# Optimization experiments

Measured on AMD Instinct MI355X. Metric: run time of the kernel, lower is better.

Reference implementation:

```python
import jax, jax.numpy as jnp
import numpy as np

N, F, T, H = 1024, 22, 1000, 64
EPS = 1e-5


def setup_inputs() -> dict:
    key = jax.random.key(0)
    ks = iter(jax.random.split(key, 64))
    def rn(shape, s=0.1):
        return jax.random.normal(next(ks), shape, jnp.float32) * s
    inp = {"x": rn((N, F, T), 1.0)}
    in_dims = [F, H, H]
    for l in range(3):
        inp[f"Wih{l}"] = rn((4 * H, in_dims[l]))
        inp[f"Whh{l}"] = rn((4 * H, H))
        inp[f"bih{l}"] = rn((4 * H,))
        inp[f"bhh{l}"] = rn((4 * H,))
    fc = [(64, 54), (54, 44), (44, 24), (24, 4)]
    for i, (di, do) in enumerate(fc):
        inp[f"w{i}"] = rn((do, di))
        inp[f"b{i}"] = rn((do,))
    for i, d in enumerate([54, 44, 24]):
        inp[f"g{i}"] = jnp.ones((d,), jnp.float32)
        inp[f"be{i}"] = jnp.zeros((d,), jnp.float32)
        inp[f"m{i}"] = rn((d,))
        inp[f"v{i}"] = jax.random.uniform(next(ks), (d,), jnp.float32) + 0.5
    return inp


def _lstm_layer(xs, Wih, Whh, b):
    # xs: (T, N, in) -> hs: (T, N, H)
    n = xs.shape[1]
    h0 = jnp.zeros((n, Whh.shape[1]), xs.dtype)
    def step(carry, xt):
        h, c = carry
        z = xt @ Wih.T + h @ Whh.T + b  # (N, 4H)
        i, f, g, o = jnp.split(z, 4, axis=-1)  # PyTorch gate order i,f,g,o
        c = jax.nn.sigmoid(f) * c + jax.nn.sigmoid(i) * jnp.tanh(g)
        h = jax.nn.sigmoid(o) * jnp.tanh(c)
        return (h, c), h
    (_, _), hs = jax.lax.scan(step, (h0, h0), xs)
    return hs


def _bn(x, g, be, m, v):
    return (x - m) * jax.lax.rsqrt(v + EPS) * g + be


def reference(x, Wih0, Whh0, bih0, bhh0, Wih1, Whh1, bih1, bhh1,
              Wih2, Whh2, bih2, bhh2,
              w0, b0, g0, be0, m0, v0,
              w1, b1, g1, be1, m1, v1,
              w2, b2, g2, be2, m2, v2,
              w3, b3):
    # (N, F, T) -> permute(0,2,1) -> (N, T, F); scan over time-major (T, N, F)
    xs = jnp.transpose(x, (2, 0, 1))
    xs = _lstm_layer(xs, Wih0, Whh0, bih0 + bhh0)
    xs = _lstm_layer(xs, Wih1, Whh1, bih1 + bhh1)
    xs = _lstm_layer(xs, Wih2, Whh2, bih2 + bhh2)
    h = xs[-1]  # last timestep, (N, H)
    h = jax.nn.relu(_bn(h @ w0.T + b0, g0, be0, m0, v0))
    h = jax.nn.relu(_bn(h @ w1.T + b1, g1, be1, m1, v1))
    h = jax.nn.relu(_bn(h @ w2.T + b2, g2, be2, m2, v2))
    return h @ w3.T + b3
```

## Files before the change

kernel.cpp:

```cpp
#include <hip/hip_runtime.h>
#include <hip/hip_fp16.h>

#define TT 1000
#define FF 22
#define HH 64
#define BB 4
#define NBLK 256
#define S0 112
#define S1 144
#define SL0 (4 * S0)
#define SL1 (4 * S1)

typedef _Float16 half8 __attribute__((ext_vector_type(8)));
typedef float float4v __attribute__((ext_vector_type(4)));

__device__ __forceinline__ float sigm(float v) {
    return __builtin_amdgcn_rcpf(1.0f + __expf(-v));
}
__device__ __forceinline__ float tanh_(float v) {
    return 1.0f - 2.0f * __builtin_amdgcn_rcpf(__expf(2.0f * v) + 1.0f);
}

__device__ __forceinline__ float sel4(const float4v a, int q) {
    float lo = (q & 2) ? a[2] : a[0];
    float hi = (q & 2) ? a[3] : a[1];
    return (q & 1) ? hi : lo;
}

__device__ __forceinline__ float gate_update(const float z[4], float& c) {
    float cc = sigm(z[1]) * c + sigm(z[0]) * tanh_(z[2]);
    c = cc;
    return sigm(z[3]) * tanh_(cc);
}

__device__ __forceinline__ int ldmin4(const int* p) {
    int4 v = *(const int4*)p;
    return min(min(v.x, v.y), min(v.z, v.w));
}

#define SPIN(cond) do { for (;;) { asm volatile("" ::: "memory"); if (cond) break; \
                        __builtin_amdgcn_s_sleep(1); } asm volatile("" ::: "memory"); } while (0)

extern "C" __global__ void __launch_bounds__(896, 1)
lstm_fused(const float* __restrict__ x,
           const float* __restrict__ Wih0, const float* __restrict__ Whh0,
           const float* __restrict__ bih0, const float* __restrict__ bhh0,
           const float* __restrict__ Wih1, const float* __restrict__ Whh1,
           const float* __restrict__ bih1, const float* __restrict__ bhh1,
           const float* __restrict__ Wih2, const float* __restrict__ Whh2,
           const float* __restrict__ bih2, const float* __restrict__ bhh2,
           const float* __restrict__ w0, const float* __restrict__ b0,
           const float* __restrict__ w1, const float* __restrict__ b1,
           const float* __restrict__ w2, const float* __restrict__ b2,
           const float* __restrict__ w3, const float* __restrict__ b3,
           const float* __restrict__ g0, const float* __restrict__ be0,
           const float* __restrict__ m0, const float* __restrict__ v0,
           const float* __restrict__ g1, const float* __restrict__ be1,
           const float* __restrict__ m1, const float* __restrict__ v1,
           const float* __restrict__ g2, const float* __restrict__ be2,
           const float* __restrict__ m2, const float* __restrict__ v2,
           float* __restrict__ out)
{
    __shared__ __align__(16) _Float16 in0[8 * SL0];
    __shared__ __align__(16) _Float16 in1[8 * SL1];
    __shared__ __align__(16) _Float16 in2[8 * SL1];
    __shared__ __align__(16) int flags[16];
    __shared__ float fcA[BB * 64];
    __shared__ float fcB[BB * 64];
    __shared__ float fcW[54 * 65];
    __shared__ float fcP[5 * 64];

    const int tid  = threadIdx.x;
    const int wv   = tid >> 6;
    const int role = wv >> 2;
    const int w4   = wv & 3;
    const int l    = tid & 63;
    const int q    = l >> 4;
    const int l15  = l & 15;
    const int u    = 16 * w4 + l15;
    const int b    = q;
    const int n0   = blockIdx.x * BB;

    for (int i = tid; i < 8 * SL0; i += 896) in0[i] = (_Float16)0.0f;
    for (int i = tid; i < 8 * SL1; i += 896) in1[i] = (_Float16)0.0f;
    for (int i = tid; i < 8 * SL1; i += 896) in2[i] = (_Float16)0.0f;
    if (tid < 16) flags[tid] = (tid >= 14) ? (1 << 29) : -1;

    half8 wf[4][4];
    float4v biasC[4];
    if (role == 2) {
#pragma unroll
        for (int g = 0; g < 4; ++g) {
            const int row = 64 * g + u;
#pragma unroll
            for (int kt = 0; kt < 3; ++kt) {
                half8 h{};
#pragma unroll
                for (int j = 0; j < 8; ++j) {
                    const int k = 32 * kt + 8 * q + j;
                    float val = 0.0f;
                    if (k < 32) { if (k < FF) val = Wih0[row * FF + k]; }
                    else        { val = Whh0[row * HH + (k - 32)]; }
                    h[j] = (_Float16)val;
                }
                wf[g][kt] = h;
            }
            float bv = bih0[row] + bhh0[row];
            biasC[g] = float4v{bv, bv, bv, bv};
        }
    } else if (role < 2) {
        const float* Wih = role ? Wih1 : Wih2;
        const float* Whh = role ? Whh1 : Whh2;
        const float* bih = role ? bih1 : bih2;
        const float* bhh = role ? bhh1 : bhh2;
#pragma unroll
        for (int g = 0; g < 4; ++g) {
            const int row = 64 * g + u;
#pragma unroll
            for (int kt = 0; kt < 4; ++kt) {
                half8 h{};
#pragma unroll
                for (int j = 0; j < 8; ++j) {
                    const int k = 32 * kt + 8 * q + j;
                    h[j] = (_Float16)((k < 64) ? Wih[row * HH + k] : Whh[row * HH + (k - 64)]);
                }
                wf[g][kt] = h;
            }
            float bv = bih[row] + bhh[row];
            biasC[g] = float4v{bv, bv, bv, bv};
        }
    }

    const int  st  = tid - 768;
    const bool xok = (role == 3) && (st >= 0) && (st < BB * FF);
    const int  xb  = xok ? (st / FF) : 0;
    const int  xf  = xok ? (st - xb * FF) : 0;
    const float* xp = x + ((size_t)(n0 + xb) * FF + xf) * TT;

    volatile int* vfl = (volatile int*)flags;
    __syncthreads();

    const int arow = (role == 2) ? ((l15 & 3) * S0 + q * 8) : ((l15 & 3) * S1 + q * 8);
    float c = 0.f;

    if (role == 3) {
        float xh = xok ? xp[0] : 0.f;
        for (int k = 0; k < 125; ++k) {
            const int tb = k * 8;
#pragma unroll
            for (int s = 0; s < 8; ++s) {
                const int t = tb + s;
                if ((s & 3) == 0) SPIN(ldmin4(flags + 8) >= t - 5);
                if (xok) in0[s * SL0 + xb * S0 + xf] = (_Float16)xh;
                __threadfence_block();
                if (l == 0) vfl[12 + (wv - 12)] = t;
                if (xok) xh = xp[(t + 1 < TT) ? (t + 1) : (TT - 1)];
            }
        }
    } else if (role == 2) {
        for (int k = 0; k < 125; ++k) {
            const int tb = k * 8;
#pragma unroll
            for (int s = 0; s < 8; ++s) {
                const int t = tb + s;
                if ((s & 3) == 0)
                    SPIN(ldmin4(flags + 12) >= t + 3 && ldmin4(flags + 4) >= t - 5);
                SPIN(ldmin4(flags + 8) >= t - 1);
                const _Float16* rd = in0 + s * SL0;
                half8 a0 = *(const half8*)(rd + arow);
                half8 a1 = *(const half8*)(rd + arow + 32);
                half8 a2 = *(const half8*)(rd + arow + 64);
                float4v acc[4];
#pragma unroll
                for (int g = 0; g < 4; ++g)
                    acc[g] = __builtin_amdgcn_mfma_f32_16x16x32_f16(a0, wf[g][0], biasC[g], 0, 0, 0);
#pragma unroll
                for (int g = 0; g < 4; ++g)
                    acc[g] = __builtin_amdgcn_mfma_f32_16x16x32_f16(a1, wf[g][1], acc[g], 0, 0, 0);
#pragma unroll
                for (int g = 0; g < 4; ++g)
                    acc[g] = __builtin_amdgcn_mfma_f32_16x16x32_f16(a2, wf[g][2], acc[g], 0, 0, 0);
                float z[4];
#pragma unroll
                for (int g = 0; g < 4; ++g) z[g] = sel4(acc[g], q);
                float h = gate_update(z, c);
                _Float16 hf = (_Float16)h;
                in0[((s + 1) & 7) * SL0 + b * S0 + 32 + u] = hf;
                in1[s * SL1 + b * S1 + u]                  = hf;
                __threadfence_block();
                if (l == 0) vfl[8 + w4] = t;
            }
        }
    } else {
        _Float16* rin  = role ? in1 : in2;
        _Float16* rout = role ? in2 : nullptr;
        const int* pin = role ? (flags + 8) : (flags + 4);
        const int* pow_ = role ? (flags + 4) : (flags + 0);
        for (int k = 0; k < 125; ++k) {
            const int tb = k * 8;
#pragma unroll
            for (int s = 0; s < 8; ++s) {
                const int t = tb + s;
                if ((s & 3) == 0) {
                    if (role) SPIN(ldmin4(pin) >= t + 3 && ldmin4(flags + 0) >= t - 5);
                    else      SPIN(ldmin4(pin) >= t + 3);
                }
                SPIN(ldmin4(pow_) >= t - 1);
                const _Float16* rd = rin + s * SL1;
                half8 a0 = *(const half8*)(rd + arow);
                half8 a1 = *(const half8*)(rd + arow + 32);
                half8 a2 = *(const half8*)(rd + arow + 64);
                half8 a3 = *(const half8*)(rd + arow + 96);
                float4v acc[4];
#pragma unroll
                for (int g = 0; g < 4; ++g)
                    acc[g] = __builtin_amdgcn_mfma_f32_16x16x32_f16(a0, wf[g][0], biasC[g], 0, 0, 0);
#pragma unroll
                for (int g = 0; g < 4; ++g)
                    acc[g] = __builtin_amdgcn_mfma_f32_16x16x32_f16(a1, wf[g][1], acc[g], 0, 0, 0);
#pragma unroll
                for (int g = 0; g < 4; ++g)
                    acc[g] = __builtin_amdgcn_mfma_f32_16x16x32_f16(a2, wf[g][2], acc[g], 0, 0, 0);
#pragma unroll
                for (int g = 0; g < 4; ++g)
                    acc[g] = __builtin_amdgcn_mfma_f32_16x16x32_f16(a3, wf[g][3], acc[g], 0, 0, 0);
                float z[4];
#pragma unroll
                for (int g = 0; g < 4; ++g) z[g] = sel4(acc[g], q);
                float h = gate_update(z, c);
                _Float16 hf = (_Float16)h;
                if (role) {
                    rin[((s + 1) & 7) * SL1 + b * S1 + 64 + u] = hf;
                    rout[s * SL1 + b * S1 + u]                 = hf;
                } else {
                    if (t != TT - 1) rin[((s + 1) & 7) * SL1 + b * S1 + 64 + u] = hf;
                    else             fcA[b * 64 + u] = h;
                }
                __threadfence_block();
                if (l == 0) vfl[(role ? 4 : 0) + w4] = t;
            }
        }
    }

    __syncthreads();

    for (int i = tid; i < 54 * 64; i += 896) fcW[(i >> 6) * 65 + (i & 63)] = w0[i];
    for (int i = tid; i < 54; i += 896) {
        fcP[i] = b0[i]; fcP[64 + i] = g0[i]; fcP[128 + i] = be0[i];
        fcP[192 + i] = m0[i]; fcP[256 + i] = v0[i];
    }
    __syncthreads();
    for (int idx = tid; idx < BB * 54; idx += 896) {
        const int bb = idx / 54, j = idx - bb * 54;
        float s = fcP[j];
        for (int k = 0; k < 64; ++k) s += fcW[j * 65 + k] * fcA[bb * 64 + k];
        s = (s - fcP[192 + j]) * rsqrtf(fcP[256 + j] + 1e-5f) * fcP[64 + j] + fcP[128 + j];
        fcB[bb * 64 + j] = fmaxf(s, 0.0f);
    }
    __syncthreads();

    for (int i = tid; i < 44 * 54; i += 896) fcW[(i / 54) * 55 + (i % 54)] = w1[i];
    for (int i = tid; i < 44; i += 896) {
        fcP[i] = b1[i]; fcP[64 + i] = g1[i]; fcP[128 + i] = be1[i];
        fcP[192 + i] = m1[i]; fcP[256 + i] = v1[i];
    }
    __syncthreads();
    for (int idx = tid; idx < BB * 44; idx += 896) {
        const int bb = idx / 44, j = idx - bb * 44;
        float s = fcP[j];
        for (int k = 0; k < 54; ++k) s += fcW[j * 55 + k] * fcB[bb * 64 + k];
        s = (s - fcP[192 + j]) * rsqrtf(fcP[256 + j] + 1e-5f) * fcP[64 + j] + fcP[128 + j];
        fcA[bb * 64 + j] = fmaxf(s, 0.0f);
    }
    __syncthreads();

    for (int i = tid; i < 24 * 44; i += 896) fcW[(i / 44) * 45 + (i % 44)] = w2[i];
    for (int i = tid; i < 24; i += 896) {
        fcP[i] = b2[i]; fcP[64 + i] = g2[i]; fcP[128 + i] = be2[i];
        fcP[192 + i] = m2[i]; fcP[256 + i] = v2[i];
    }
    __syncthreads();
    for (int idx = tid; idx < BB * 24; idx += 896) {
        const int bb = idx / 24, j = idx - bb * 24;
        float s = fcP[j];
        for (int k = 0; k < 44; ++k) s += fcW[j * 45 + k] * fcA[bb * 64 + k];
        s = (s - fcP[192 + j]) * rsqrtf(fcP[256 + j] + 1e-5f) * fcP[64 + j] + fcP[128 + j];
        fcB[bb * 64 + j] = fmaxf(s, 0.0f);
    }
    __syncthreads();

    for (int i = tid; i < 4 * 24; i += 896) fcW[(i / 24) * 25 + (i % 24)] = w3[i];
    for (int i = tid; i < 4; i += 896) fcP[i] = b3[i];
    __syncthreads();
    for (int idx = tid; idx < BB * 4; idx += 896) {
        const int bb = idx / 4, j = idx - bb * 4;
        float s = fcP[j];
        for (int k = 0; k < 24; ++k) s += fcW[j * 25 + k] * fcB[bb * 64 + k];
        out[(size_t)(n0 + bb) * 4 + j] = s;
    }
}

extern "C" void kernel_launch(void* const* d_in, const int* in_sizes, int n_in,
                              void* d_out, int out_size, void* d_ws, size_t ws_size,
                              hipStream_t stream) {
    const float* p[33];
    for (int i = 0; i < 33; ++i) p[i] = (const float*)d_in[i];
    lstm_fused<<<NBLK, 896, 0, stream>>>(
        p[0],
        p[1], p[2], p[3], p[4],
        p[5], p[6], p[7], p[8],
        p[9], p[10], p[11], p[12],
        p[13], p[14], p[15], p[16], p[17], p[18], p[19], p[20],
        p[21], p[22], p[23], p[24],
        p[25], p[26], p[27], p[28],
        p[29], p[30], p[31], p[32],
        (float*)d_out);
}
```

Before: 819.4 us.

## Replace flag-based spin synchronization with lockstep block barriers per wavefront step

Removes the shared-memory flag counters and spin-wait loops between the x-loader, layer0, layer1 and layer2 wave groups. All roles now advance in a skewed wavefront schedule (layer l processes timestep tau-l), separated by one s_barrier per step after an LDS wait. This trades the polling and sleep latency of the flag protocol for a full workgroup barrier every step, which forces every role to wait for the slowest one at each step.

```diff
diff --git a/kernel.cpp b/kernel.cpp
--- a/kernel.cpp
+++ b/kernel.cpp
@@ -33,13 +33,8 @@
     return sigm(z[3]) * tanh_(cc);
 }
 
-__device__ __forceinline__ int ldmin4(const int* p) {
-    int4 v = *(const int4*)p;
-    return min(min(v.x, v.y), min(v.z, v.w));
-}
-
-#define SPIN(cond) do { for (;;) { asm volatile("" ::: "memory"); if (cond) break; \
-                        __builtin_amdgcn_s_sleep(1); } asm volatile("" ::: "memory"); } while (0)
+#define LFENCE() asm volatile("s_waitcnt lgkmcnt(0)" ::: "memory")
+#define BAR()    __builtin_amdgcn_s_barrier()
 
 extern "C" __global__ void __launch_bounds__(896, 1)
 lstm_fused(const float* __restrict__ x,
@@ -64,7 +59,6 @@
     __shared__ __align__(16) _Float16 in0[8 * SL0];
     __shared__ __align__(16) _Float16 in1[8 * SL1];
     __shared__ __align__(16) _Float16 in2[8 * SL1];
-    __shared__ __align__(16) int flags[16];
     __shared__ float fcA[BB * 64];
     __shared__ float fcB[BB * 64];
     __shared__ float fcW[54 * 65];
@@ -84,7 +78,6 @@
     for (int i = tid; i < 8 * SL0; i += 896) in0[i] = (_Float16)0.0f;
     for (int i = tid; i < 8 * SL1; i += 896) in1[i] = (_Float16)0.0f;
     for (int i = tid; i < 8 * SL1; i += 896) in2[i] = (_Float16)0.0f;
-    if (tid < 16) flags[tid] = (tid >= 14) ? (1 << 29) : -1;
 
     half8 wf[4][4];
     float4v biasC[4];
@@ -137,107 +130,115 @@
     const int  xf  = xok ? (st - xb * FF) : 0;
     const float* xp = x + ((size_t)(n0 + xb) * FF + xf) * TT;
 
-    volatile int* vfl = (volatile int*)flags;
-    __syncthreads();
+    __syncthreads();
+
+    if (xok) in0[0 * SL0 + xb * S0 + xf] = (_Float16)xp[0];
+    float xA = xok ? xp[1] : 0.f;
+    float xB = xok ? xp[2] : 0.f;
 
     const int arow = (role == 2) ? ((l15 & 3) * S0 + q * 8) : ((l15 & 3) * S1 + q * 8);
     float c = 0.f;
 
-    if (role == 3) {
-        float xh = xok ? xp[0] : 0.f;
-        for (int k = 0; k < 125; ++k) {
-            const int tb = k * 8;
-#pragma unroll
-            for (int s = 0; s < 8; ++s) {
-                const int t = tb + s;
-                if ((s & 3) == 0) SPIN(ldmin4(flags + 8) >= t - 5);
-                if (xok) in0[s * SL0 + xb * S0 + xf] = (_Float16)xh;
-                __threadfence_block();
-                if (l == 0) vfl[12 + (wv - 12)] = t;
-                if (xok) xh = xp[(t + 1 < TT) ? (t + 1) : (TT - 1)];
-            }
-        }
-    } else if (role == 2) {
-        for (int k = 0; k < 125; ++k) {
-            const int tb = k * 8;
-#pragma unroll
-            for (int s = 0; s < 8; ++s) {
-                const int t = tb + s;
-                if ((s & 3) == 0)
-                    SPIN(ldmin4(flags + 12) >= t + 3 && ldmin4(flags + 4) >= t - 5);
-                SPIN(ldmin4(flags + 8) >= t - 1);
-                const _Float16* rd = in0 + s * SL0;
-                half8 a0 = *(const half8*)(rd + arow);
-                half8 a1 = *(const half8*)(rd + arow + 32);
-                half8 a2 = *(const half8*)(rd + arow + 64);
-                float4v acc[4];
-#pragma unroll
-                for (int g = 0; g < 4; ++g)
-                    acc[g] = __builtin_amdgcn_mfma_f32_16x16x32_f16(a0, wf[g][0], biasC[g], 0, 0, 0);
-#pragma unroll
-                for (int g = 0; g < 4; ++g)
-                    acc[g] = __builtin_amdgcn_mfma_f32_16x16x32_f16(a1, wf[g][1], acc[g], 0, 0, 0);
-#pragma unroll
-                for (int g = 0; g < 4; ++g)
-                    acc[g] = __builtin_amdgcn_mfma_f32_16x16x32_f16(a2, wf[g][2], acc[g], 0, 0, 0);
-                float z[4];
-#pragma unroll
-                for (int g = 0; g < 4; ++g) z[g] = sel4(acc[g], q);
-                float h = gate_update(z, c);
-                _Float16 hf = (_Float16)h;
-                in0[((s + 1) & 7) * SL0 + b * S0 + 32 + u] = hf;
-                in1[s * SL1 + b * S1 + u]                  = hf;
-                __threadfence_block();
-                if (l == 0) vfl[8 + w4] = t;
-            }
-        }
-    } else {
-        _Float16* rin  = role ? in1 : in2;
-        _Float16* rout = role ? in2 : nullptr;
-        const int* pin = role ? (flags + 8) : (flags + 4);
-        const int* pow_ = role ? (flags + 4) : (flags + 0);
-        for (int k = 0; k < 125; ++k) {
-            const int tb = k * 8;
-#pragma unroll
-            for (int s = 0; s < 8; ++s) {
-                const int t = tb + s;
-                if ((s & 3) == 0) {
-                    if (role) SPIN(ldmin4(pin) >= t + 3 && ldmin4(flags + 0) >= t - 5);
-                    else      SPIN(ldmin4(pin) >= t + 3);
-                }
-                SPIN(ldmin4(pow_) >= t - 1);
-                const _Float16* rd = rin + s * SL1;
-                half8 a0 = *(const half8*)(rd + arow);
-                half8 a1 = *(const half8*)(rd + arow + 32);
-                half8 a2 = *(const half8*)(rd + arow + 64);
-                half8 a3 = *(const half8*)(rd + arow + 96);
-                float4v acc[4];
-#pragma unroll
-                for (int g = 0; g < 4; ++g)
-                    acc[g] = __builtin_amdgcn_mfma_f32_16x16x32_f16(a0, wf[g][0], biasC[g], 0, 0, 0);
-#pragma unroll
-                for (int g = 0; g < 4; ++g)
-                    acc[g] = __builtin_amdgcn_mfma_f32_16x16x32_f16(a1, wf[g][1], acc[g], 0, 0, 0);
-#pragma unroll
-                for (int g = 0; g < 4; ++g)
-                    acc[g] = __builtin_amdgcn_mfma_f32_16x16x32_f16(a2, wf[g][2], acc[g], 0, 0, 0);
-#pragma unroll
-                for (int g = 0; g < 4; ++g)
-                    acc[g] = __builtin_amdgcn_mfma_f32_16x16x32_f16(a3, wf[g][3], acc[g], 0, 0, 0);
-                float z[4];
-#pragma unroll
-                for (int g = 0; g < 4; ++g) z[g] = sel4(acc[g], q);
-                float h = gate_update(z, c);
-                _Float16 hf = (_Float16)h;
-                if (role) {
-                    rin[((s + 1) & 7) * SL1 + b * S1 + 64 + u] = hf;
-                    rout[s * SL1 + b * S1 + u]                 = hf;
-                } else {
-                    if (t != TT - 1) rin[((s + 1) & 7) * SL1 + b * S1 + 64 + u] = hf;
-                    else             fcA[b * 64 + u] = h;
-                }
-                __threadfence_block();
-                if (l == 0) vfl[(role ? 4 : 0) + w4] = t;
+    for (int k = 0; k < 126; ++k) {
+#pragma unroll
+        for (int s = 0; s < 8; ++s) {
+            const int tau = 8 * k + s;
+            LFENCE();
+            BAR();
+
+            if (role == 3) {
+                if (tau <= TT - 2) {
+                    if (xok) in0[((s + 1) & 7) * SL0 + xb * S0 + xf] = (_Float16)xA;
+                    xA = xB;
+                    if (xok) {
+                        int tn = tau + 3; if (tn > TT - 1) tn = TT - 1;
+                        xB = xp[tn];
+                    }
+                }
+            } else if (role == 2) {
+                if (tau <= TT - 1) {
+                    const _Float16* rd = in0 + s * SL0;
+                    half8 a0 = *(const half8*)(rd + arow);
+                    half8 a1 = *(const half8*)(rd + arow + 32);
+                    half8 a2 = *(const half8*)(rd + arow + 64);
+                    float4v acc[4];
+#pragma unroll
+                    for (int g = 0; g < 4; ++g)
+                        acc[g] = __builtin_amdgcn_mfma_f32_16x16x32_f16(a0, wf[g][0], biasC[g], 0, 0, 0);
+#pragma unroll
+                    for (int g = 0; g < 4; ++g)
+                        acc[g] = __builtin_amdgcn_mfma_f32_16x16x32_f16(a1, wf[g][1], acc[g], 0, 0, 0);
+#pragma unroll
+                    for (int g = 0; g < 4; ++g)
+                        acc[g] = __builtin_amdgcn_mfma_f32_16x16x32_f16(a2, wf[g][2], acc[g], 0, 0, 0);
+                    float z[4];
+#pragma unroll
+                    for (int g = 0; g < 4; ++g) z[g] = sel4(acc[g], q);
+                    float h = gate_update(z, c);
+                    _Float16 hf = (_Float16)h;
+                    in0[((s + 1) & 7) * SL0 + b * S0 + 32 + u] = hf;
+                    in1[s * SL1 + b * S1 + u]                  = hf;
+                }
+            } else if (role == 1) {
+                if (tau >= 1 && tau <= TT) {
+                    const int sr = (s + 7) & 7;
+                    const _Float16* rd = in1 + sr * SL1;
+                    half8 a0 = *(const half8*)(rd + arow);
+                    half8 a1 = *(const half8*)(rd + arow + 32);
+                    half8 a2 = *(const half8*)(rd + arow + 64);
+                    half8 a3 = *(const half8*)(rd + arow + 96);
+                    float4v acc[4];
+#pragma unroll
+                    for (int g = 0; g < 4; ++g)
+                        acc[g] = __builtin_amdgcn_mfma_f32_16x16x32_f16(a0, wf[g][0], biasC[g], 0, 0, 0);
+#pragma unroll
+                    for (int g = 0; g < 4; ++g)
+                        acc[g] = __builtin_amdgcn_mfma_f32_16x16x32_f16(a1, wf[g][1], acc[g], 0, 0, 0);
+#pragma unroll
+                    for (int g = 0; g < 4; ++g)
+                        acc[g] = __builtin_amdgcn_mfma_f32_16x16x32_f16(a2, wf[g][2], acc[g], 0, 0, 0);
+#pragma unroll
+                    for (int g = 0; g < 4; ++g)
+                        acc[g] = __builtin_amdgcn_mfma_f32_16x16x32_f16(a3, wf[g][3], acc[g], 0, 0, 0);
+                    float z[4];
+#pragma unroll
+                    for (int g = 0; g < 4; ++g) z[g] = sel4(acc[g], q);
+                    float h = gate_update(z, c);
+                    _Float16 hf = (_Float16)h;
+                    in1[s * SL1 + b * S1 + 64 + u] = hf;
+                    in2[sr * SL1 + b * S1 + u]     = hf;
+                }
+            } else {
+                if (tau >= 2 && tau <= TT + 1) {
+                    const int sr = (s + 6) & 7;
+                    const _Float16* rd = in2 + sr * SL1;
+                    half8 a0 = *(const half8*)(rd + arow);
+                    half8 a1 = *(const half8*)(rd + arow + 32);
+                    half8 a2 = *(const half8*)(rd + arow + 64);
+                    half8 a3 = *(const half8*)(rd + arow + 96);
+                    float4v acc[4];
+#pragma unroll
+                    for (int g = 0; g < 4; ++g)
+                        acc[g] = __builtin_amdgcn_mfma_f32_16x16x32_f16(a0, wf[g][0], biasC[g], 0, 0, 0);
+#pragma unroll
+                    for (int g = 0; g < 4; ++g)
+                        acc[g] = __builtin_amdgcn_mfma_f32_16x16x32_f16(a1, wf[g][1], acc[g], 0, 0, 0);
+#pragma unroll
+                    for (int g = 0; g < 4; ++g)
+                        acc[g] = __builtin_amdgcn_mfma_f32_16x16x32_f16(a2, wf[g][2], acc[g], 0, 0, 0);
+#pragma unroll
+                    for (int g = 0; g < 4; ++g)
+                        acc[g] = __builtin_amdgcn_mfma_f32_16x16x32_f16(a3, wf[g][3], acc[g], 0, 0, 0);
+                    float z[4];
+#pragma unroll
+                    for (int g = 0; g < 4; ++g) z[g] = sel4(acc[g], q);
+                    float h = gate_update(z, c);
+                    if (tau != TT + 1) {
+                        in2[((s + 7) & 7) * SL1 + b * S1 + 64 + u] = (_Float16)h;
+                    } else {
+                        fcA[b * 64 + u] = h;
+                    }
+                }
             }
         }
     }
```

New measurement: 783.8 us. -4.3%, faster.
